# Optimization experiments

Hardware: AMD Instinct MI355X
Metric: run time of the kernel (lower is better)

The kernel has to match this reference:

```python
import jax, jax.numpy as jnp
import numpy as np

N_NODES = 100000
N_EDGES = 1600000
D = 128            # in_channels == hidden_channels
N_CLASSES = 10
N_GRAPHS = 512
N_CONVS = 3        # num_layers - 1


def _linear_params(key, d_in, d_out):
    kw, kb = jax.random.split(key)
    bound = 1.0 / np.sqrt(d_in)
    w = jax.random.uniform(kw, (d_in, d_out), jnp.float32, -bound, bound)
    b = jax.random.uniform(kb, (d_out,), jnp.float32, -bound, bound)
    return w, b


def setup_inputs() -> dict:
    key = jax.random.key(0)
    ks = jax.random.split(key, 16)
    x = jax.random.normal(ks[0], (N_NODES, D), jnp.float32)
    edge_index = jax.random.randint(ks[1], (2, N_EDGES), 0, N_NODES, jnp.int64)
    batch = jnp.sort(jax.random.randint(ks[2], (N_NODES,), 0, N_GRAPHS, jnp.int64))
    inp = {"x": x, "edge_index": edge_index, "batch": batch}
    # 3 GIN convs, each an MLP: Linear(D,D) -> ReLU -> Linear(D,D)
    for i in range(N_CONVS):
        w1, b1 = _linear_params(ks[3 + 2 * i], D, D)
        w2, b2 = _linear_params(ks[4 + 2 * i], D, D)
        inp[f"w1_{i}"], inp[f"b1_{i}"] = w1, b1
        inp[f"w2_{i}"], inp[f"b2_{i}"] = w2, b2
    wl, bl = _linear_params(ks[10], D, N_CLASSES)
    inp["w_lin"], inp["b_lin"] = wl, bl
    return inp


def _gin_conv(x, src, dst, w1, b1, w2, b2):
    # sum_{j->i} x_j  (scatter-add over edges), eps = 0 (PyG default)
    agg = jax.ops.segment_sum(x[src], dst, num_segments=N_NODES)
    h = agg + x  # (1 + eps) * x + aggregate
    h = jax.nn.relu(h @ w1 + b1) @ w2 + b2  # nn.Sequential MLP
    return h


def reference(x, edge_index, batch,
              w1_0, b1_0, w2_0, b2_0,
              w1_1, b1_1, w2_1, b2_1,
              w1_2, b1_2, w2_2, b2_2,
              w_lin, b_lin):
    src, dst = edge_index[0], edge_index[1]
    params = [(w1_0, b1_0, w2_0, b2_0),
              (w1_1, b1_1, w2_1, b2_1),
              (w1_2, b1_2, w2_2, b2_2)]
    for (w1, b1, w2, b2) in params:
        x = _gin_conv(x, src, dst, w1, b1, w2, b2)
        x = jax.nn.relu(x)
    pooled = jax.ops.segment_sum(x, batch, num_segments=N_GRAPHS)  # global_add_pool
    return pooled @ w_lin + b_lin
```

## Files before the change

kernel.cpp:

```cpp
#include <hip/hip_runtime.h>
#include <hip/hip_bf16.h>

#define N_NODES 100000
#define N_EDGES 1600000
#define DIM 128
#define N_GRAPHS 512
#define N_CLASSES 10
#define SCAN_CHUNK 1024

#define NBK 782
#define EB 8192
#define NEB 196
#define HN (NBK * NEB)
#define NCH_HIST ((HN + SCAN_CHUNK - 1) / SCAN_CHUNK)
#define NCH_CNT ((N_NODES + SCAN_CHUNK - 1) / SCAN_CHUNK)

#define POOL_CHUNK 128
#define NPB ((N_NODES + POOL_CHUNK - 1) / POOL_CHUNK)

typedef __attribute__((ext_vector_type(8))) short short8;
typedef __attribute__((ext_vector_type(4))) float floatx4;

__device__ __forceinline__ uint bfround(float f) {
    uint u = __builtin_bit_cast(uint, f);
    return (u + 0x7fffu + ((u >> 16) & 1u)) >> 16;
}
__device__ __forceinline__ float bflo(uint u) { return __builtin_bit_cast(float, u << 16); }
__device__ __forceinline__ float bfhi(uint u) { return __builtin_bit_cast(float, u & 0xffff0000u); }

__device__ __forceinline__ void addrow(float* a, uint4 v) {
    a[0] += bflo(v.x); a[1] += bfhi(v.x);
    a[2] += bflo(v.y); a[3] += bfhi(v.y);
    a[4] += bflo(v.z); a[5] += bfhi(v.z);
    a[6] += bflo(v.w); a[7] += bfhi(v.w);
}


__global__ void k_cvt_x(const float* __restrict__ x, ushort* __restrict__ xb, int n4) {
    int i = blockIdx.x * blockDim.x + threadIdx.x;
    int stride = gridDim.x * blockDim.x;
    for (; i < n4; i += stride) {
        floatx4 v = *(const floatx4*)(x + (size_t)i * 4);
        ushort4 o;
        o.x = (ushort)bfround(v.x);
        o.y = (ushort)bfround(v.y);
        o.z = (ushort)bfround(v.z);
        o.w = (ushort)bfround(v.w);
        *(ushort4*)(xb + (size_t)i * 4) = o;
    }
}

struct WPtrs { const float* w[6]; };

__global__ __launch_bounds__(256) void k_cvt_w(WPtrs wp, ushort* __restrict__ Wt) {
    int m = blockIdx.x >> 6;
    int idx = (blockIdx.x & 63) * 256 + threadIdx.x;
    int n = idx >> 7, k = idx & 127;
    Wt[(size_t)m * 16384 + idx] = (ushort)bfround(wp.w[m][k * 128 + n]);
}


__global__ void k_zero(int* __restrict__ p, int n) {
    int i = blockIdx.x * blockDim.x + threadIdx.x;
    int stride = gridDim.x * blockDim.x;
    for (; i < n; i += stride) p[i] = 0;
}

__global__ __launch_bounds__(256) void k_hist(const int* __restrict__ dstv,
                                              int* __restrict__ hist) {
    __shared__ int cnt[NBK];
    int blk = blockIdx.x, tid = threadIdx.x;
    for (int i = tid; i < NBK; i += 256) cnt[i] = 0;
    __syncthreads();
    int base = blk * EB;
    int end = min(base + EB, N_EDGES);
    for (int i = base + tid; i < end; i += 256) atomicAdd(&cnt[dstv[i] >> 7], 1);
    __syncthreads();
    for (int b = tid; b < NBK; b += 256) hist[b * NEB + blk] = cnt[b];
}

__global__ __launch_bounds__(256) void k_reduce(const int* __restrict__ src, int n,
                                                int* __restrict__ chunk_sums) {
    int base = blockIdx.x * SCAN_CHUNK;
    int tid = threadIdx.x;
    int s = 0;
    for (int i = tid; i < SCAN_CHUNK; i += 256) {
        int idx = base + i;
        if (idx < n) s += src[idx];
    }
    __shared__ int red[256];
    red[tid] = s;
    __syncthreads();
    for (int off = 128; off > 0; off >>= 1) {
        if (tid < off) red[tid] += red[tid + off];
        __syncthreads();
    }
    if (tid == 0) chunk_sums[blockIdx.x] = red[0];
}

__global__ __launch_bounds__(256) void k_scan_c(int* __restrict__ chunk_sums, int nch,
                                                int* __restrict__ total_out) {
    __shared__ int sm[256];
    int tid = threadIdx.x;
    int v = (tid < nch) ? chunk_sums[tid] : 0;
    sm[tid] = v;
    __syncthreads();
    for (int off = 1; off < 256; off <<= 1) {
        int t = (tid >= off) ? sm[tid - off] : 0;
        __syncthreads();
        sm[tid] += t;
        __syncthreads();
    }
    if (tid < nch) chunk_sums[tid] = sm[tid] - v;
    if (tid == 255) *total_out = sm[255];
}

__global__ __launch_bounds__(256) void k_apply(const int* __restrict__ src,
                                               const int* __restrict__ chunk_sums,
                                               int* __restrict__ dst, int n) {
    int base = blockIdx.x * SCAN_CHUNK;
    int tid = threadIdx.x;
    int i0 = base + tid * 4;
    int v[4];
    int s = 0;
    #pragma unroll
    for (int j = 0; j < 4; j++) {
        int idx = i0 + j;
        v[j] = (idx < n) ? src[idx] : 0;
        s += v[j];
    }
    __shared__ int sc[256];
    sc[tid] = s;
    __syncthreads();
    for (int off = 1; off < 256; off <<= 1) {
        int t = (tid >= off) ? sc[tid - off] : 0;
        __syncthreads();
        sc[tid] += t;
        __syncthreads();
    }
    int excl = sc[tid] - s + chunk_sums[blockIdx.x];
    #pragma unroll
    for (int j = 0; j < 4; j++) {
        int idx = i0 + j;
        if (idx < n) dst[idx] = excl;
        excl += v[j];
    }
}

__global__ __launch_bounds__(256) void k_scatter(const int* __restrict__ srcv,
                                                 const int* __restrict__ dstv,
                                                 const int* __restrict__ hists,
                                                 uint* __restrict__ sorted) {
    __shared__ int cur[NBK];
    int blk = blockIdx.x, tid = threadIdx.x;
    for (int b = tid; b < NBK; b += 256) cur[b] = hists[b * NEB + blk];
    __syncthreads();
    int base = blk * EB;
    int end = min(base + EB, N_EDGES);
    for (int i = base + tid; i < end; i += 256) {
        int s = srcv[i], d = dstv[i];
        int p = atomicAdd(&cur[d >> 7], 1);
        sorted[p] = (uint)s | ((uint)(d & 127) << 17);
    }
}

__global__ __launch_bounds__(256) void k_bcount_s(const int* __restrict__ hists,
                                                  const uint* __restrict__ sorted,
                                                  int* __restrict__ counts) {
    __shared__ int cnt[128];
    int b = blockIdx.x, tid = threadIdx.x;
    if (tid < 128) cnt[tid] = 0;
    __syncthreads();
    int s0 = hists[b * NEB];
    int s1 = (b == NBK - 1) ? N_EDGES : hists[(b + 1) * NEB];
    for (int i = s0 + tid; i < s1; i += 256) atomicAdd(&cnt[(sorted[i] >> 17) & 127], 1);
    __syncthreads();
    int node = (b << 7) + tid;
    if (tid < 128 && node < N_NODES) counts[node] = cnt[tid];
}

__global__ __launch_bounds__(256) void k_fill_s(const int* __restrict__ hists,
                                                const uint* __restrict__ sorted,
                                                const int* __restrict__ row_ptr,
                                                int* __restrict__ col) {
    __shared__ int cur[128];
    int b = blockIdx.x, tid = threadIdx.x;
    int node = (b << 7) + tid;
    if (tid < 128 && node < N_NODES) cur[tid] = row_ptr[node];
    __syncthreads();
    int s0 = hists[b * NEB];
    int s1 = (b == NBK - 1) ? N_EDGES : hists[(b + 1) * NEB];
    for (int i = s0 + tid; i < s1; i += 256) {
        uint e = sorted[i];
        int p = atomicAdd(&cur[(e >> 17) & 127], 1);
        col[p] = (int)(e & 0x1FFFFu);
    }
}

__global__ __launch_bounds__(256) void k_agg(const uint4* __restrict__ xr,
                                             const int* __restrict__ row_ptr,
                                             const int* __restrict__ col,
                                             uint4* __restrict__ hr) {
    int wv = threadIdx.x >> 6;
    int nA = blockIdx.x * 8 + wv * 2;
    if (nA >= N_NODES) return;
    int nB = nA + 1;
    bool hasB = nB < N_NODES;
    int lane = threadIdx.x & 63;
    int grp = lane >> 4;
    int l16 = lane & 15;

    float accA[8], accB[8];
    #pragma unroll
    for (int i = 0; i < 8; i++) { accA[i] = 0.f; accB[i] = 0.f; }
    if (grp == 0) {
        uint4 sv = xr[(size_t)nA * 16 + l16];
        accA[0] = bflo(sv.x); accA[1] = bfhi(sv.x);
        accA[2] = bflo(sv.y); accA[3] = bfhi(sv.y);
        accA[4] = bflo(sv.z); accA[5] = bfhi(sv.z);
        accA[6] = bflo(sv.w); accA[7] = bfhi(sv.w);
    } else if (grp == 1 && hasB) {
        uint4 sv = xr[(size_t)nB * 16 + l16];
        accB[0] = bflo(sv.x); accB[1] = bfhi(sv.x);
        accB[2] = bflo(sv.y); accB[3] = bfhi(sv.y);
        accB[4] = bflo(sv.z); accB[5] = bfhi(sv.z);
        accB[6] = bflo(sv.w); accB[7] = bfhi(sv.w);
    }

    int jA = row_ptr[nA], eA = row_ptr[nA + 1];
    int jB = hasB ? row_ptr[nB] : 0;
    int eB = hasB ? row_ptr[nB + 1] : 0;

    while (jA < eA || jB < eB) {
        int chunkA = eA - jA; chunkA = chunkA < 0 ? 0 : (chunkA > 64 ? 64 : chunkA);
        int chunkB = eB - jB; chunkB = chunkB < 0 ? 0 : (chunkB > 64 ? 64 : chunkB);
        int myA = (lane < chunkA) ? col[jA + lane] : 0;
        int myB = (lane < chunkB) ? col[jB + lane] : 0;
        int cm = chunkA > chunkB ? chunkA : chunkB;
        int iters = (cm + 15) >> 4;
        for (int f = 0; f < iters; f++) {
            int p = (f << 4) + grp;
            int a0 = __shfl(myA, (p      < chunkA) ? p      : 0);
            int a1 = __shfl(myA, (p + 4  < chunkA) ? p + 4  : 0);
            int a2 = __shfl(myA, (p + 8  < chunkA) ? p + 8  : 0);
            int a3 = __shfl(myA, (p + 12 < chunkA) ? p + 12 : 0);
            int b0 = __shfl(myB, (p      < chunkB) ? p      : 0);
            int b1 = __shfl(myB, (p + 4  < chunkB) ? p + 4  : 0);
            int b2 = __shfl(myB, (p + 8  < chunkB) ? p + 8  : 0);
            int b3 = __shfl(myB, (p + 12 < chunkB) ? p + 12 : 0);
            uint4 vA0 = xr[(size_t)a0 * 16 + l16];
            uint4 vA1 = xr[(size_t)a1 * 16 + l16];
            uint4 vA2 = xr[(size_t)a2 * 16 + l16];
            uint4 vA3 = xr[(size_t)a3 * 16 + l16];
            uint4 vB0 = xr[(size_t)b0 * 16 + l16];
            uint4 vB1 = xr[(size_t)b1 * 16 + l16];
            uint4 vB2 = xr[(size_t)b2 * 16 + l16];
            uint4 vB3 = xr[(size_t)b3 * 16 + l16];
            if (p < chunkA)      addrow(accA, vA0);
            if (p + 4 < chunkA)  addrow(accA, vA1);
            if (p + 8 < chunkA)  addrow(accA, vA2);
            if (p + 12 < chunkA) addrow(accA, vA3);
            if (p < chunkB)      addrow(accB, vB0);
            if (p + 4 < chunkB)  addrow(accB, vB1);
            if (p + 8 < chunkB)  addrow(accB, vB2);
            if (p + 12 < chunkB) addrow(accB, vB3);
        }
        jA += 64; jB += 64;
    }

    #pragma unroll
    for (int i = 0; i < 8; i++) {
        accA[i] += __shfl_xor(accA[i], 16);
        accA[i] += __shfl_xor(accA[i], 32);
        accB[i] += __shfl_xor(accB[i], 16);
        accB[i] += __shfl_xor(accB[i], 32);
    }

    if (grp == 0) {
        uint4 o;
        o.x = bfround(accA[0]) | (bfround(accA[1]) << 16);
        o.y = bfround(accA[2]) | (bfround(accA[3]) << 16);
        o.z = bfround(accA[4]) | (bfround(accA[5]) << 16);
        o.w = bfround(accA[6]) | (bfround(accA[7]) << 16);
        hr[(size_t)nA * 16 + l16] = o;
    } else if (grp == 1 && hasB) {
        uint4 o;
        o.x = bfround(accB[0]) | (bfround(accB[1]) << 16);
        o.y = bfround(accB[2]) | (bfround(accB[3]) << 16);
        o.z = bfround(accB[4]) | (bfround(accB[5]) << 16);
        o.w = bfround(accB[6]) | (bfround(accB[7]) << 16);
        hr[(size_t)nB * 16 + l16] = o;
    }
}

__device__ __forceinline__ int loff(int row, int byte) {
    return row * 256 + (byte ^ ((row & 7) << 4));
}

__global__ __launch_bounds__(256) void k_mlp(const ushort* __restrict__ hin,
                                             ushort* __restrict__ xout,
                                             const ushort* __restrict__ W1t,
                                             const float* __restrict__ b1,
                                             const ushort* __restrict__ W2t,
                                             const float* __restrict__ b2) {
    __shared__ alignas(16) char hT[64 * 256];
    int tid = threadIdx.x;
    int lane = tid & 63;
    int wave = tid >> 6;
    int node0 = blockIdx.x * 64;
    int l15 = lane & 15;
    int lhi = lane >> 4;
    int ncol0 = wave * 32;

    #pragma unroll
    for (int it = 0; it < 4; ++it) {
        int idx = it * 256 + tid;
        int row = idx >> 4;
        int cb = (idx & 15) * 16;
        int gn = node0 + row;
        floatx4 v = {0.f, 0.f, 0.f, 0.f};
        if (gn < N_NODES) v = *(const floatx4*)(hin + (size_t)gn * 128 + cb / 2);
        *(floatx4*)(hT + loff(row, cb)) = v;
    }
    __syncthreads();

    short8 bf[4][2];
    #pragma unroll
    for (int ks = 0; ks < 4; ks++)
        #pragma unroll
        for (int nf = 0; nf < 2; nf++) {
            int nrow = ncol0 + nf * 16 + l15;
            bf[ks][nf] = *(const short8*)(W1t + nrow * 128 + ks * 32 + lhi * 8);
        }

    floatx4 acc[4][2];
    #pragma unroll
    for (int m = 0; m < 4; m++)
        #pragma unroll
        for (int nf = 0; nf < 2; nf++) {
            float bias = b1[ncol0 + nf * 16 + l15];
            acc[m][nf] = (floatx4){bias, bias, bias, bias};
        }

    #pragma unroll
    for (int ks = 0; ks < 4; ks++) {
        short8 af[4];
        #pragma unroll
        for (int m = 0; m < 4; m++)
            af[m] = *(const short8*)(hT + loff(m * 16 + l15, ks * 64 + lhi * 16));
        #pragma unroll
        for (int m = 0; m < 4; m++)
            #pragma unroll
            for (int nf = 0; nf < 2; nf++)
                acc[m][nf] = __builtin_amdgcn_mfma_f32_16x16x32_bf16(af[m], bf[ks][nf], acc[m][nf], 0, 0, 0);
    }
    __syncthreads();

    #pragma unroll
    for (int m = 0; m < 4; m++)
        #pragma unroll
        for (int nf = 0; nf < 2; nf++) {
            int colb = (ncol0 + nf * 16 + l15) * 2;
            #pragma unroll
            for (int j = 0; j < 4; j++) {
                int row = m * 16 + lhi * 4 + j;
                float t = acc[m][nf][j];
                t = t > 0.f ? t : 0.f;
                *(ushort*)(hT + loff(row, colb)) = (ushort)bfround(t);
            }
        }
    __syncthreads();

    #pragma unroll
    for (int ks = 0; ks < 4; ks++)
        #pragma unroll
        for (int nf = 0; nf < 2; nf++) {
            int nrow = ncol0 + nf * 16 + l15;
            bf[ks][nf] = *(const short8*)(W2t + nrow * 128 + ks * 32 + lhi * 8);
        }
    #pragma unroll
    for (int m = 0; m < 4; m++)
        #pragma unroll
        for (int nf = 0; nf < 2; nf++) {
            float bias = b2[ncol0 + nf * 16 + l15];
            acc[m][nf] = (floatx4){bias, bias, bias, bias};
        }

    #pragma unroll
    for (int ks = 0; ks < 4; ks++) {
        short8 af[4];
        #pragma unroll
        for (int m = 0; m < 4; m++)
            af[m] = *(const short8*)(hT + loff(m * 16 + l15, ks * 64 + lhi * 16));
        #pragma unroll
        for (int m = 0; m < 4; m++)
            #pragma unroll
            for (int nf = 0; nf < 2; nf++)
                acc[m][nf] = __builtin_amdgcn_mfma_f32_16x16x32_bf16(af[m], bf[ks][nf], acc[m][nf], 0, 0, 0);
    }
    __syncthreads();

    #pragma unroll
    for (int m = 0; m < 4; m++)
        #pragma unroll
        for (int nf = 0; nf < 2; nf++) {
            int colb = (ncol0 + nf * 16 + l15) * 2;
            #pragma unroll
            for (int j = 0; j < 4; j++) {
                int row = m * 16 + lhi * 4 + j;
                float t = acc[m][nf][j];
                t = t > 0.f ? t : 0.f;
                *(ushort*)(hT + loff(row, colb)) = (ushort)bfround(t);
            }
        }
    __syncthreads();
    #pragma unroll
    for (int it = 0; it < 4; ++it) {
        int idx = it * 256 + tid;
        int row = idx >> 4;
        int cb = (idx & 15) * 16;
        int gn = node0 + row;
        if (gn < N_NODES)
            *(floatx4*)(xout + (size_t)gn * 128 + cb / 2) = *(const floatx4*)(hT + loff(row, cb));
    }
}

__global__ __launch_bounds__(256) void k_pool(const uint* __restrict__ x,
                                              const int* __restrict__ batch,
                                              float* __restrict__ pooled) {
    int n0 = blockIdx.x * POOL_CHUNK;
    int wave = threadIdx.x >> 6;
    int lane = threadIdx.x & 63;
    float a0 = 0.f, a1 = 0.f;
    int cur = -1;
    int endn = min(n0 + POOL_CHUNK, N_NODES);
    for (int n = n0 + wave; n < endn; n += 4) {
        int g = batch[n];
        if (g != cur) {
            if (cur >= 0) {
                atomicAdd(&pooled[cur * 128 + lane * 2], a0);
                atomicAdd(&pooled[cur * 128 + lane * 2 + 1], a1);
            }
            cur = g; a0 = 0.f; a1 = 0.f;
        }
        uint v = x[(size_t)n * 64 + lane];
        a0 += bflo(v); a1 += bfhi(v);
    }
    if (cur >= 0) {
        atomicAdd(&pooled[cur * 128 + lane * 2], a0);
        atomicAdd(&pooled[cur * 128 + lane * 2 + 1], a1);
    }
}

__global__ __launch_bounds__(64) void k_final(const float* __restrict__ pooled,
                                              const float* __restrict__ wl,
                                              const float* __restrict__ bl,
                                              float* __restrict__ out) {
    int g = blockIdx.x;
    int o = threadIdx.x;
    if (o >= N_CLASSES) return;
    float acc = bl[o];
    for (int k = 0; k < 128; k++) acc += pooled[g * 128 + k] * wl[k * N_CLASSES + o];
    out[g * N_CLASSES + o] = acc;
}


extern "C" void kernel_launch(void* const* d_in, const int* in_sizes, int n_in,
                              void* d_out, int out_size, void* d_ws, size_t ws_size,
                              hipStream_t stream) {
    const float* x0  = (const float*)d_in[0];
    const int* ei    = (const int*)d_in[1];
    const int* batch = (const int*)d_in[2];
    const float* W1[3] = {(const float*)d_in[3], (const float*)d_in[7],  (const float*)d_in[11]};
    const float* B1[3] = {(const float*)d_in[4], (const float*)d_in[8],  (const float*)d_in[12]};
    const float* W2[3] = {(const float*)d_in[5], (const float*)d_in[9],  (const float*)d_in[13]};
    const float* B2[3] = {(const float*)d_in[6], (const float*)d_in[10], (const float*)d_in[14]};
    const float* wl = (const float*)d_in[15];
    const float* bl = (const float*)d_in[16];
    float* out = (float*)d_out;

    const int* srcv = ei;
    const int* dstv = ei + N_EDGES;

    char* w = (char*)d_ws;
    ushort* xb = (ushort*)w;
    ushort* hb = xb + (size_t)N_NODES * DIM;
    ushort* wt = hb + (size_t)N_NODES * DIM;
    float* pooled = (float*)(wt + 6 * 128 * 128);
    int* row_ptr = (int*)(pooled + N_GRAPHS * DIM);
    int* counts  = row_ptr + (N_NODES + 2);
    int* colidx  = counts + N_NODES;
    int* chunk_sums = colidx + N_EDGES;
    int* hist    = chunk_sums + 256;
    uint* sorted = (uint*)(hist + HN + 1);

    hipLaunchKernelGGL(k_cvt_x, dim3(2048), dim3(256), 0, stream, x0, xb, N_NODES * DIM / 4);
    WPtrs wp;
    wp.w[0] = W1[0]; wp.w[1] = W2[0]; wp.w[2] = W1[1];
    wp.w[3] = W2[1]; wp.w[4] = W1[2]; wp.w[5] = W2[2];
    hipLaunchKernelGGL(k_cvt_w, dim3(6 * 64), dim3(256), 0, stream, wp, wt);
    hipLaunchKernelGGL(k_zero, dim3(64), dim3(256), 0, stream, (int*)pooled, N_GRAPHS * DIM);

    hipLaunchKernelGGL(k_hist, dim3(NEB), dim3(256), 0, stream, dstv, hist);
    hipLaunchKernelGGL(k_reduce, dim3(NCH_HIST), dim3(256), 0, stream, hist, HN, chunk_sums);
    hipLaunchKernelGGL(k_scan_c, dim3(1), dim3(256), 0, stream, chunk_sums, NCH_HIST, hist + HN);
    hipLaunchKernelGGL(k_apply, dim3(NCH_HIST), dim3(256), 0, stream, hist, chunk_sums, hist, HN);
    hipLaunchKernelGGL(k_scatter, dim3(NEB), dim3(256), 0, stream, srcv, dstv, hist, sorted);
    hipLaunchKernelGGL(k_bcount_s, dim3(NBK), dim3(256), 0, stream, hist, sorted, counts);
    hipLaunchKernelGGL(k_reduce, dim3(NCH_CNT), dim3(256), 0, stream, counts, N_NODES, chunk_sums);
    hipLaunchKernelGGL(k_scan_c, dim3(1), dim3(256), 0, stream, chunk_sums, NCH_CNT, row_ptr + N_NODES);
    hipLaunchKernelGGL(k_apply, dim3(NCH_CNT), dim3(256), 0, stream, counts, chunk_sums, row_ptr, N_NODES);
    hipLaunchKernelGGL(k_fill_s, dim3(NBK), dim3(256), 0, stream, hist, sorted, row_ptr, colidx);

    dim3 aggGrid((N_NODES + 7) / 8), aggBlk(256);
    dim3 mlpGrid((N_NODES + 63) / 64), mlpBlk(256);
    for (int l = 0; l < 3; l++) {
        hipLaunchKernelGGL(k_agg, aggGrid, aggBlk, 0, stream,
                           (const uint4*)xb, row_ptr, colidx, (uint4*)hb);
        hipLaunchKernelGGL(k_mlp, mlpGrid, mlpBlk, 0, stream,
                           hb, xb, wt + (size_t)(2 * l) * 16384, B1[l],
                           wt + (size_t)(2 * l + 1) * 16384, B2[l]);
    }

    hipLaunchKernelGGL(k_pool, dim3(NPB), dim3(256), 0, stream, (const uint*)xb, batch, pooled);
    hipLaunchKernelGGL(k_final, dim3(N_GRAPHS), dim3(64), 0, stream, pooled, wl, bl, out);
}
```

Before: 344.9 us.

## Fuse CSR build kernels and merge conversion/zeroing into fewer launches

Merges the per-bucket count, the global count scan and the fill into one k_build kernel. It does this by computing row_ptr from the bucket offset already held in the histogram plus an in-block scan of the 128 node counts. It also folds weight conversion into the x conversion kernel and the zeroing of pooled into k_hist. The aim is to remove six kernel launches and the serial dependencies between them, at the cost of a slightly longer CSR build kernel.

```diff
diff --git a/kernel.cpp b/kernel.cpp
--- a/kernel.cpp
+++ b/kernel.cpp
@@ -13,7 +13,6 @@
 #define NEB 196
 #define HN (NBK * NEB)
 #define NCH_HIST ((HN + SCAN_CHUNK - 1) / SCAN_CHUNK)
-#define NCH_CNT ((N_NODES + SCAN_CHUNK - 1) / SCAN_CHUNK)
 
 #define POOL_CHUNK 128
 #define NPB ((N_NODES + POOL_CHUNK - 1) / POOL_CHUNK)
@@ -35,11 +34,13 @@
     a[6] += bflo(v.w); a[7] += bfhi(v.w);
 }
 
-
-__global__ void k_cvt_x(const float* __restrict__ x, ushort* __restrict__ xb, int n4) {
-    int i = blockIdx.x * blockDim.x + threadIdx.x;
+struct WPtrs { const float* w[6]; };
+
+__global__ void k_cvt_x(const float* __restrict__ x, ushort* __restrict__ xb,
+                        WPtrs wp, ushort* __restrict__ wt) {
     int stride = gridDim.x * blockDim.x;
-    for (; i < n4; i += stride) {
+    int t0 = blockIdx.x * blockDim.x + threadIdx.x;
+    for (int i = t0; i < N_NODES * DIM / 4; i += stride) {
         floatx4 v = *(const floatx4*)(x + (size_t)i * 4);
         ushort4 o;
         o.x = (ushort)bfround(v.x);
@@ -48,26 +49,20 @@
         o.w = (ushort)bfround(v.w);
         *(ushort4*)(xb + (size_t)i * 4) = o;
     }
-}
-
-struct WPtrs { const float* w[6]; };
-
-__global__ __launch_bounds__(256) void k_cvt_w(WPtrs wp, ushort* __restrict__ Wt) {
-    int m = blockIdx.x >> 6;
-    int idx = (blockIdx.x & 63) * 256 + threadIdx.x;
-    int n = idx >> 7, k = idx & 127;
-    Wt[(size_t)m * 16384 + idx] = (ushort)bfround(wp.w[m][k * 128 + n]);
-}
-
-
-__global__ void k_zero(int* __restrict__ p, int n) {
-    int i = blockIdx.x * blockDim.x + threadIdx.x;
-    int stride = gridDim.x * blockDim.x;
-    for (; i < n; i += stride) p[i] = 0;
-}
+    for (int j = t0; j < 6 * 16384; j += stride) {
+        int m = j >> 14, idx = j & 16383;
+        int n = idx >> 7, k = idx & 127;
+        wt[j] = (ushort)bfround(wp.w[m][k * 128 + n]);
+    }
+}
+
 
 __global__ __launch_bounds__(256) void k_hist(const int* __restrict__ dstv,
-                                              int* __restrict__ hist) {
+                                              int* __restrict__ hist,
+                                              float* __restrict__ pooled) {
+    int gt = blockIdx.x * 256 + threadIdx.x;
+    for (int i = gt; i < N_GRAPHS * DIM; i += NEB * 256) pooled[i] = 0.f;
+
     __shared__ int cnt[NBK];
     int blk = blockIdx.x, tid = threadIdx.x;
     for (int i = tid; i < NBK; i += 256) cnt[i] = 0;
@@ -98,8 +93,7 @@
     if (tid == 0) chunk_sums[blockIdx.x] = red[0];
 }
 
-__global__ __launch_bounds__(256) void k_scan_c(int* __restrict__ chunk_sums, int nch,
-                                                int* __restrict__ total_out) {
+__global__ __launch_bounds__(256) void k_scan_c(int* __restrict__ chunk_sums, int nch) {
     __shared__ int sm[256];
     int tid = threadIdx.x;
     int v = (tid < nch) ? chunk_sums[tid] : 0;
@@ -112,7 +106,6 @@
         __syncthreads();
     }
     if (tid < nch) chunk_sums[tid] = sm[tid] - v;
-    if (tid == 255) *total_out = sm[255];
 }
 
 __global__ __launch_bounds__(256) void k_apply(const int* __restrict__ src,
@@ -164,10 +157,13 @@
     }
 }
 
-__global__ __launch_bounds__(256) void k_bcount_s(const int* __restrict__ hists,
-                                                  const uint* __restrict__ sorted,
-                                                  int* __restrict__ counts) {
+__global__ __launch_bounds__(256) void k_build(const int* __restrict__ hists,
+                                               const uint* __restrict__ sorted,
+                                               int* __restrict__ row_ptr,
+                                               int* __restrict__ col) {
     __shared__ int cnt[128];
+    __shared__ int scn[128];
+    __shared__ int cur[128];
     int b = blockIdx.x, tid = threadIdx.x;
     if (tid < 128) cnt[tid] = 0;
     __syncthreads();
@@ -175,21 +171,22 @@
     int s1 = (b == NBK - 1) ? N_EDGES : hists[(b + 1) * NEB];
     for (int i = s0 + tid; i < s1; i += 256) atomicAdd(&cnt[(sorted[i] >> 17) & 127], 1);
     __syncthreads();
+    if (tid < 128) scn[tid] = cnt[tid];
+    __syncthreads();
+    for (int off = 1; off < 128; off <<= 1) {
+        int t = (tid < 128 && tid >= off) ? scn[tid - off] : 0;
+        __syncthreads();
+        if (tid < 128) scn[tid] += t;
+        __syncthreads();
+    }
     int node = (b << 7) + tid;
-    if (tid < 128 && node < N_NODES) counts[node] = cnt[tid];
-}
-
-__global__ __launch_bounds__(256) void k_fill_s(const int* __restrict__ hists,
-                                                const uint* __restrict__ sorted,
-                                                const int* __restrict__ row_ptr,
-                                                int* __restrict__ col) {
-    __shared__ int cur[128];
-    int b = blockIdx.x, tid = threadIdx.x;
-    int node = (b << 7) + tid;
-    if (tid < 128 && node < N_NODES) cur[tid] = row_ptr[node];
-    __syncthreads();
-    int s0 = hists[b * NEB];
-    int s1 = (b == NBK - 1) ? N_EDGES : hists[(b + 1) * NEB];
+    if (tid < 128) {
+        int excl = s0 + scn[tid] - cnt[tid];
+        cur[tid] = excl;
+        if (node < N_NODES) row_ptr[node] = excl;
+    }
+    if (b == 0 && tid == 0) row_ptr[N_NODES] = N_EDGES;
+    __syncthreads();
     for (int i = s0 + tid; i < s1; i += 256) {
         uint e = sorted[i];
         int p = atomicAdd(&cur[(e >> 17) & 127], 1);
@@ -488,29 +485,22 @@
     ushort* wt = hb + (size_t)N_NODES * DIM;
     float* pooled = (float*)(wt + 6 * 128 * 128);
     int* row_ptr = (int*)(pooled + N_GRAPHS * DIM);
-    int* counts  = row_ptr + (N_NODES + 2);
-    int* colidx  = counts + N_NODES;
+    int* colidx  = row_ptr + (N_NODES + 2);
     int* chunk_sums = colidx + N_EDGES;
     int* hist    = chunk_sums + 256;
     uint* sorted = (uint*)(hist + HN + 1);
 
-    hipLaunchKernelGGL(k_cvt_x, dim3(2048), dim3(256), 0, stream, x0, xb, N_NODES * DIM / 4);
     WPtrs wp;
     wp.w[0] = W1[0]; wp.w[1] = W2[0]; wp.w[2] = W1[1];
     wp.w[3] = W2[1]; wp.w[4] = W1[2]; wp.w[5] = W2[2];
-    hipLaunchKernelGGL(k_cvt_w, dim3(6 * 64), dim3(256), 0, stream, wp, wt);
-    hipLaunchKernelGGL(k_zero, dim3(64), dim3(256), 0, stream, (int*)pooled, N_GRAPHS * DIM);
-
-    hipLaunchKernelGGL(k_hist, dim3(NEB), dim3(256), 0, stream, dstv, hist);
+    hipLaunchKernelGGL(k_cvt_x, dim3(2048), dim3(256), 0, stream, x0, xb, wp, wt);
+
+    hipLaunchKernelGGL(k_hist, dim3(NEB), dim3(256), 0, stream, dstv, hist, pooled);
     hipLaunchKernelGGL(k_reduce, dim3(NCH_HIST), dim3(256), 0, stream, hist, HN, chunk_sums);
-    hipLaunchKernelGGL(k_scan_c, dim3(1), dim3(256), 0, stream, chunk_sums, NCH_HIST, hist + HN);
+    hipLaunchKernelGGL(k_scan_c, dim3(1), dim3(256), 0, stream, chunk_sums, NCH_HIST);
     hipLaunchKernelGGL(k_apply, dim3(NCH_HIST), dim3(256), 0, stream, hist, chunk_sums, hist, HN);
     hipLaunchKernelGGL(k_scatter, dim3(NEB), dim3(256), 0, stream, srcv, dstv, hist, sorted);
-    hipLaunchKernelGGL(k_bcount_s, dim3(NBK), dim3(256), 0, stream, hist, sorted, counts);
-    hipLaunchKernelGGL(k_reduce, dim3(NCH_CNT), dim3(256), 0, stream, counts, N_NODES, chunk_sums);
-    hipLaunchKernelGGL(k_scan_c, dim3(1), dim3(256), 0, stream, chunk_sums, NCH_CNT, row_ptr + N_NODES);
-    hipLaunchKernelGGL(k_apply, dim3(NCH_CNT), dim3(256), 0, stream, counts, chunk_sums, row_ptr, N_NODES);
-    hipLaunchKernelGGL(k_fill_s, dim3(NBK), dim3(256), 0, stream, hist, sorted, row_ptr, colidx);
+    hipLaunchKernelGGL(k_build, dim3(NBK), dim3(256), 0, stream, hist, sorted, row_ptr, colidx);
 
     dim3 aggGrid((N_NODES + 7) / 8), aggBlk(256);
     dim3 mlpGrid((N_NODES + 63) / 64), mlpBlk(256);
```

New measurement: 330.6 us. -4.1%, faster.
